# Performance work log

Measured on AMD Instinct MI355X. Metric: run time of the kernel, lower is better.

The kernel has to match this reference:

```python
import jax, jax.numpy as jnp
from jax import lax
import numpy as np

N_INPUTS = 2048
UNITS = 2048
L = 8
FANIN = 4096
TOTAL = N_INPUTS + L * UNITS  # 18432, size of flattened outputs vector


def setup_inputs() -> dict:
    key = jax.random.key(0)
    k1, k2, k3, k4 = jax.random.split(key, 4)
    x = jax.random.normal(k1, (N_INPUTS,), dtype=jnp.float32)
    node_inds = jax.random.randint(k2, (L, FANIN), 0, TOTAL, dtype=jnp.int32)
    # 0.02 scale keeps tanh out of deep saturation (matches small evolved weights)
    Ws = jax.random.normal(k3, (L, FANIN, UNITS), dtype=jnp.float32) * 0.02
    bs = jax.random.normal(k4, (L, UNITS), dtype=jnp.float32) * 0.02
    return {"x": x, "node_inds": node_inds, "Ws": Ws, "bs": bs}


def reference(x, node_inds, Ws, bs):
    # Flattened shared state vector, zero-initialized like the tf.Variable.
    outputs = jnp.zeros((TOTAL,), dtype=x.dtype)
    start = 0  # static python offset: out_update_inds are contiguous ranges
    for i in range(L):
        # scatter_nd_update of x into contiguous slice == dynamic_update_slice
        outputs = lax.dynamic_update_slice(outputs, x, (start,))
        start += x.shape[0]
        # gather node-specific indices then tiny Dense + tanh
        gathered = jnp.take(outputs, node_inds[i])          # [FANIN]
        x = jnp.tanh(gathered @ Ws[i] + bs[i])              # [UNITS]
    return x
```

## Files before the change

### kernel.cpp

```cpp
#include <hip/hip_runtime.h>
#include <cmath>

#define N_INPUTS 2048
#define UNITS    2048
#define L_LAYERS 8
#define FANIN    4096
#define TOTAL    18432

#define NTHREADS 256
#define RK       16
#define KC       (FANIN / RK)
#define JTILE    1024
#define P_BLOCKS (2 * KC)

__device__ __forceinline__ float col_reduce(const float* __restrict__ P, int col)
{
    int lane = threadIdx.x & 63;
    float s = 0.f;
    #pragma unroll
    for (int m = 0; m < KC / 64; ++m)
        s += P[(size_t)(lane + m * 64) * UNITS + col];
    #pragma unroll
    for (int off = 32; off; off >>= 1)
        s += __shfl_down(s, off, 64);
    return __shfl(s, 0, 64);
}

__global__ __launch_bounds__(NTHREADS) void layer_kernel(
    int layer,
    const float* __restrict__ x,
    const int*   __restrict__ node_inds,
    const float* __restrict__ Ws,
    const float* __restrict__ bs,
    float*       __restrict__ outputs,
    const float* __restrict__ Pprev,
    float*       __restrict__ Pcur)
{
    const int b    = blockIdx.x;
    const int t    = threadIdx.x;
    const int wv   = t >> 6;
    const int lane = t & 63;
    const int jhalf = b & 1;
    const int kc    = b >> 1;

    __shared__ float gsh[RK];

    {
        int col = b * 4 + wv;
        if (layer == 0) {
            if (lane == 0) outputs[col] = x[col];
        } else {
            float s = col_reduce(Pprev, col);
            float y = tanhf(s + bs[(layer - 1) * UNITS + col]);
            if (lane == 0) outputs[(size_t)layer * UNITS + col] = y;
        }
    }

    #pragma unroll
    for (int j = 0; j < 4; ++j) {
        int q   = wv * 4 + j;
        int idx = node_inds[layer * FANIN + kc * RK + q];
        float g;
        if (layer == 0) {
            g = (idx < N_INPUTS) ? x[idx] : 0.f;
        } else if (idx < layer * UNITS) {
            g = outputs[idx];
        } else if (idx < (layer + 1) * UNITS) {
            int col = idx - layer * UNITS;
            float s = col_reduce(Pprev, col);
            g = tanhf(s + bs[(layer - 1) * UNITS + col]);
        } else {
            g = 0.f;
        }
        if (lane == 0) gsh[q] = g;
    }
    __syncthreads();

    const int jbase = jhalf * JTILE + t * 4;
    const float4* W4 = (const float4*)(
        Ws + ((size_t)layer * FANIN + (size_t)kc * RK) * UNITS + jbase);

    float4 a; a.x = 0.f; a.y = 0.f; a.z = 0.f; a.w = 0.f;
    #pragma unroll
    for (int k = 0; k < RK; ++k) {
        float  g = gsh[k];
        float4 w = W4[(size_t)k * (UNITS / 4)];
        a.x += g * w.x; a.y += g * w.y; a.z += g * w.z; a.w += g * w.w;
    }
    *(float4*)(Pcur + (size_t)kc * UNITS + jbase) = a;
}

__global__ __launch_bounds__(NTHREADS) void tail_kernel(
    const float* __restrict__ Pprev,
    const float* __restrict__ bs,
    float*       __restrict__ out)
{
    int wv   = threadIdx.x >> 6;
    int lane = threadIdx.x & 63;
    int col  = blockIdx.x * 4 + wv;
    float s = col_reduce(Pprev, col);
    float y = tanhf(s + bs[(L_LAYERS - 1) * UNITS + col]);
    if (lane == 0) out[col] = y;
}

extern "C" void kernel_launch(void* const* d_in, const int* in_sizes, int n_in,
                              void* d_out, int out_size, void* d_ws, size_t ws_size,
                              hipStream_t stream) {
    const float* x         = (const float*)d_in[0];
    const int*   node_inds = (const int*)  d_in[1];
    const float* Ws        = (const float*)d_in[2];
    const float* bs        = (const float*)d_in[3];
    float*       out       = (float*)d_out;
    float*       ws        = (float*)d_ws;

    float* outputs = ws;
    float* P0      = ws + TOTAL;
    float* P1      = P0 + (size_t)KC * UNITS;

    float* pbuf[2] = { P0, P1 };

    for (int i = 0; i < L_LAYERS; ++i) {
        layer_kernel<<<P_BLOCKS, NTHREADS, 0, stream>>>(
            i, x, node_inds, Ws, bs, outputs,
            pbuf[(i + 1) & 1],
            pbuf[i & 1]);
    }
    tail_kernel<<<UNITS / 4, NTHREADS, 0, stream>>>(
        pbuf[(L_LAYERS - 1) & 1], bs, out);
}
```

Measured before the change: 417.8 us.

## Restructure split-K GEMV to 8-way K split with in-block reduction and compact partials

```diff
diff --git a/kernel.cpp b/kernel.cpp
--- a/kernel.cpp
+++ b/kernel.cpp
@@ -8,25 +8,15 @@
 #define TOTAL    18432
 
 #define NTHREADS 256
-#define RK       16
-#define KC       (FANIN / RK)
-#define JTILE    1024
-#define P_BLOCKS (2 * KC)
+#define KSPLIT   8
+#define RKB      (FANIN / KSPLIT)
+#define JT       16
+#define JG       (UNITS / JT)
+#define P_BLOCKS (KSPLIT * JG)
+#define PSTRIDE  (KSPLIT * JT)
 
-__device__ __forceinline__ float col_reduce(const float* __restrict__ P, int col)
-{
-    int lane = threadIdx.x & 63;
-    float s = 0.f;
-    #pragma unroll
-    for (int m = 0; m < KC / 64; ++m)
-        s += P[(size_t)(lane + m * 64) * UNITS + col];
-    #pragma unroll
-    for (int off = 32; off; off >>= 1)
-        s += __shfl_down(s, off, 64);
-    return __shfl(s, 0, 64);
-}
 
-__global__ __launch_bounds__(NTHREADS) void layer_kernel(
+__global__ __launch_bounds__(NTHREADS, 4) void layer_kernel(
     int layer,
     const float* __restrict__ x,
     const int*   __restrict__ node_inds,
@@ -36,71 +26,106 @@
     const float* __restrict__ Pprev,
     float*       __restrict__ Pcur)
 {
-    const int b    = blockIdx.x;
-    const int t    = threadIdx.x;
-    const int wv   = t >> 6;
-    const int lane = t & 63;
-    const int jhalf = b & 1;
-    const int kc    = b >> 1;
+    const int b  = blockIdx.x;
+    const int t  = threadIdx.x;
+    const int jg = b & (JG - 1);
+    const int kc = b >> 7;
+    const int j0 = jg * JT;
+    const int k0 = kc * RKB;
+    const int c4 = t & 3;
+    const int rr = t >> 2;
 
-    __shared__ float gsh[RK];
+    __shared__ float  gsh[RKB];
+    __shared__ float4 redsh[4][4];
 
-    {
-        int col = b * 4 + wv;
+    const float* Wb = Ws + ((size_t)layer * FANIN + k0) * UNITS + j0 + c4 * 4;
+    float4 w[8];
+    #pragma unroll
+    for (int i = 0; i < 8; ++i)
+        w[i] = *(const float4*)(Wb + (size_t)(rr + 64 * i) * UNITS);
+
+    #pragma unroll
+    for (int h = 0; h < 2; ++h) {
+        int r   = t + h * NTHREADS;
+        int idx = node_inds[layer * FANIN + k0 + r];
+        float v;
         if (layer == 0) {
-            if (lane == 0) outputs[col] = x[col];
+            v = (idx < N_INPUTS) ? x[idx] : 0.f;
+        } else if (idx < layer * UNITS) {
+            v = outputs[idx];
+        } else if (idx < (layer + 1) * UNITS) {
+            int col = idx - layer * UNITS;
+            const float* pp = Pprev + (col >> 4) * PSTRIDE + (col & 15);
+            float s = 0.f;
+            #pragma unroll
+            for (int q = 0; q < KSPLIT; ++q) s += pp[q * JT];
+            v = tanhf(s + bs[(layer - 1) * UNITS + col]);
         } else {
-            float s = col_reduce(Pprev, col);
-            float y = tanhf(s + bs[(layer - 1) * UNITS + col]);
-            if (lane == 0) outputs[(size_t)layer * UNITS + col] = y;
+            v = 0.f;
         }
+        gsh[r] = v;
+    }
+
+    if (kc == 0 && t < JT) {
+        int col = j0 + t;
+        float y;
+        if (layer == 0) {
+            y = x[col];
+        } else {
+            const float* pp = Pprev + jg * PSTRIDE + t;
+            float s = 0.f;
+            #pragma unroll
+            for (int q = 0; q < KSPLIT; ++q) s += pp[q * JT];
+            y = tanhf(s + bs[(layer - 1) * UNITS + col]);
+        }
+        outputs[(size_t)layer * UNITS + col] = y;
+    }
+
+    __syncthreads();
+
+    float4 a; a.x = 0.f; a.y = 0.f; a.z = 0.f; a.w = 0.f;
+    #pragma unroll
+    for (int i = 0; i < 8; ++i) {
+        float g = gsh[rr + 64 * i];
+        a.x += g * w[i].x; a.y += g * w[i].y;
+        a.z += g * w[i].z; a.w += g * w[i].w;
     }
 
     #pragma unroll
-    for (int j = 0; j < 4; ++j) {
-        int q   = wv * 4 + j;
-        int idx = node_inds[layer * FANIN + kc * RK + q];
-        float g;
-        if (layer == 0) {
-            g = (idx < N_INPUTS) ? x[idx] : 0.f;
-        } else if (idx < layer * UNITS) {
-            g = outputs[idx];
-        } else if (idx < (layer + 1) * UNITS) {
-            int col = idx - layer * UNITS;
-            float s = col_reduce(Pprev, col);
-            g = tanhf(s + bs[(layer - 1) * UNITS + col]);
-        } else {
-            g = 0.f;
-        }
-        if (lane == 0) gsh[q] = g;
+    for (int off = 4; off <= 32; off <<= 1) {
+        a.x += __shfl_xor(a.x, off, 64);
+        a.y += __shfl_xor(a.y, off, 64);
+        a.z += __shfl_xor(a.z, off, 64);
+        a.w += __shfl_xor(a.w, off, 64);
     }
+    const int wv   = t >> 6;
+    const int lane = t & 63;
+    if (lane < 4) redsh[wv][lane] = a;
     __syncthreads();
 
-    const int jbase = jhalf * JTILE + t * 4;
-    const float4* W4 = (const float4*)(
-        Ws + ((size_t)layer * FANIN + (size_t)kc * RK) * UNITS + jbase);
-
-    float4 a; a.x = 0.f; a.y = 0.f; a.z = 0.f; a.w = 0.f;
-    #pragma unroll
-    for (int k = 0; k < RK; ++k) {
-        float  g = gsh[k];
-        float4 w = W4[(size_t)k * (UNITS / 4)];
-        a.x += g * w.x; a.y += g * w.y; a.z += g * w.z; a.w += g * w.w;
+    if (t < 4) {
+        float4 s0 = redsh[0][t], s1 = redsh[1][t];
+        float4 s2 = redsh[2][t], s3 = redsh[3][t];
+        float4 s;
+        s.x = (s0.x + s1.x) + (s2.x + s3.x);
+        s.y = (s0.y + s1.y) + (s2.y + s3.y);
+        s.z = (s0.z + s1.z) + (s2.z + s3.z);
+        s.w = (s0.w + s1.w) + (s2.w + s3.w);
+        *(float4*)(Pcur + jg * PSTRIDE + kc * JT + t * 4) = s;
     }
-    *(float4*)(Pcur + (size_t)kc * UNITS + jbase) = a;
 }
 
 __global__ __launch_bounds__(NTHREADS) void tail_kernel(
-    const float* __restrict__ Pprev,
+    const float* __restrict__ P,
     const float* __restrict__ bs,
     float*       __restrict__ out)
 {
-    int wv   = threadIdx.x >> 6;
-    int lane = threadIdx.x & 63;
-    int col  = blockIdx.x * 4 + wv;
-    float s = col_reduce(Pprev, col);
-    float y = tanhf(s + bs[(L_LAYERS - 1) * UNITS + col]);
-    if (lane == 0) out[col] = y;
+    int col = blockIdx.x * NTHREADS + threadIdx.x;
+    const float* pp = P + (col >> 4) * PSTRIDE + (col & 15);
+    float s = 0.f;
+    #pragma unroll
+    for (int q = 0; q < KSPLIT; ++q) s += pp[q * JT];
+    out[col] = tanhf(s + bs[(L_LAYERS - 1) * UNITS + col]);
 }
 
 extern "C" void kernel_launch(void* const* d_in, const int* in_sizes, int n_in,
@@ -115,8 +140,7 @@
 
     float* outputs = ws;
     float* P0      = ws + TOTAL;
-    float* P1      = P0 + (size_t)KC * UNITS;
-
+    float* P1      = P0 + (size_t)JG * PSTRIDE;
     float* pbuf[2] = { P0, P1 };
 
     for (int i = 0; i < L_LAYERS; ++i) {
@@ -125,6 +149,6 @@
             pbuf[(i + 1) & 1],
             pbuf[i & 1]);
     }
-    tail_kernel<<<UNITS / 4, NTHREADS, 0, stream>>>(
+    tail_kernel<<<UNITS / NTHREADS, NTHREADS, 0, stream>>>(
         pbuf[(L_LAYERS - 1) & 1], bs, out);
 }
```

Result: faster. 405.1 us (-3.0%).
